# Optimization experiments

Measured on AMD Instinct MI355X. Metric: run time of the kernel, lower is better.

## Reference

```python
import jax, jax.numpy as jnp
import numpy as np

B, T, C = 1, 2048, 1024
E = 32            # n_routed_experts
TOPK = 4
H = 512           # expert_hidden_size
HS = 1024         # shared hidden: round_up(2*512, 256)
ROUTE_SCALE = 1.0


def setup_inputs() -> dict:
    key = jax.random.key(0)
    ks = jax.random.split(key, 6)
    s = 0.02  # init scale for stable logits/activations
    return {
        "x": jax.random.normal(ks[0], (B, T, C), jnp.float32),
        "gate_w": jax.random.normal(ks[1], (C, E), jnp.float32) * s,
        "gate_bias": jnp.zeros((E,), jnp.float32),
        "shared_gate_w": jax.random.normal(ks[2], (C, 2 * HS), jnp.float32) * s,
        "shared_down_w": jax.random.normal(ks[3], (HS, C), jnp.float32) * s,
        "expert_gate_w": jax.random.normal(ks[4], (E, C, 2 * H), jnp.float32) * s,
        "expert_down_w": jax.random.normal(ks[5], (E, H, C), jnp.float32) * s,
    }


def _swiglu(x, gate_w, down_w):
    # torch: y, gate = chunk(gate_proj(x), 2); down(silu(gate) * y)
    u = x @ gate_w
    y, g = jnp.split(u, 2, axis=-1)
    return (jax.nn.silu(g) * y) @ down_w


def reference(x, gate_w, gate_bias, shared_gate_w, shared_down_w,
              expert_gate_w, expert_down_w):
    Bx, Tx, Cx = x.shape
    xf = x.reshape(-1, Cx)                     # (N, C)
    N = xf.shape[0]

    # shared expert (always active)
    shared = _swiglu(x, shared_gate_w, shared_down_w)   # (B, T, C)

    # sigmoid top-k gate with load-balance bias (bias only affects selection)
    scores = jax.nn.sigmoid(xf @ gate_w)                # (N, E)
    _, topk_idx = jax.lax.top_k(scores + gate_bias, TOPK)
    w = jnp.take_along_axis(scores, topk_idx, axis=-1)  # (N, K)
    w = w / jnp.sum(w, axis=-1, keepdims=True) * ROUTE_SCALE

    # dense combine weights: combine[n, e] = routing weight of expert e for token n (0 if unselected)
    combine = jnp.zeros((N, E), xf.dtype).at[jnp.arange(N)[:, None], topk_idx].add(w)

    # routed experts: masked dense evaluation (math identical to permute + grouped GEMM + scatter-combine)
    out = jnp.zeros_like(xf)
    for e in range(E):
        out = out + combine[:, e:e + 1] * _swiglu(xf, expert_gate_w[e], expert_down_w[e])

    return shared + out.reshape(Bx, Tx, Cx)
```

## Files before the change

### kernel.cpp

```cpp
#include <hip/hip_runtime.h>
#include <hip/hip_bf16.h>
#include <math.h>

#define N_TOK 2048
#define C_DIM 1024
#define E_NUM 32
#define TOPKK 4
#define H_EXP 512
#define HS_SH 1024
#define NSLOT (N_TOK * TOPKK)

typedef __attribute__((ext_vector_type(8))) short short8;
typedef __attribute__((ext_vector_type(4))) float f32x4;

__device__ __forceinline__ ushort f2b(float f) {
    __hip_bfloat16 h = __float2bfloat16(f);
    return *(ushort*)&h;
}
__device__ __forceinline__ float silu_f(float g) { return g / (1.f + __expf(-g)); }

__device__ __forceinline__ void glds16(const ushort* g, ushort* l) {
    __builtin_amdgcn_global_load_lds(
        (const __attribute__((address_space(1))) unsigned int*)g,
        (__attribute__((address_space(3))) unsigned int*)l, 16, 0, 0);
}

__global__ __launch_bounds__(256) void router_kernel(
    const float* __restrict__ x, const float* __restrict__ gate_w,
    const float* __restrict__ gate_bias, ushort* __restrict__ xb,
    int* __restrict__ topk_idx, float* __restrict__ topk_w)
{
    __shared__ float xs[C_DIM];
    __shared__ float part[8][E_NUM];
    __shared__ float scores_s[E_NUM];
    const int n = blockIdx.x;
    const int t = threadIdx.x;
    const float* xr = x + (size_t)n * C_DIM;
    {
        float4 v = ((const float4*)xr)[t];
        xs[t * 4 + 0] = v.x; xs[t * 4 + 1] = v.y;
        xs[t * 4 + 2] = v.z; xs[t * 4 + 3] = v.w;
        ushort4 o;
        o.x = f2b(v.x); o.y = f2b(v.y); o.z = f2b(v.z); o.w = f2b(v.w);
        ((ushort4*)(xb + (size_t)n * C_DIM))[t] = o;
    }
    __syncthreads();
    const int e = t & 31, cp = t >> 5;
    float s = 0.f;
#pragma unroll 4
    for (int c = cp * 128; c < cp * 128 + 128; ++c)
        s += xs[c] * gate_w[c * E_NUM + e];
    part[cp][e] = s;
    __syncthreads();
    if (t < E_NUM) {
        float tot = 0.f;
#pragma unroll
        for (int i = 0; i < 8; ++i) tot += part[i][t];
        scores_s[t] = 1.f / (1.f + expf(-tot));
    }
    __syncthreads();
    if (t < 64) {
        const int l = t;
        const float sc  = (l < E_NUM) ? scores_s[l] : -INFINITY;
        const float scb = (l < E_NUM) ? sc + gate_bias[l] : -INFINITY;
        bool used = false;
        int myidx[TOPKK]; float myw[TOPKK]; float wsum = 0.f;
#pragma unroll
        for (int k = 0; k < TOPKK; ++k) {
            float v = used ? -INFINITY : scb;
            float m = v;
#pragma unroll
            for (int d = 1; d < 64; d <<= 1) m = fmaxf(m, __shfl_xor(m, d));
            unsigned long long b = __ballot(v == m);
            const int pick = __ffsll((unsigned long long)b) - 1;
            if (l == pick) used = true;
            const float w = __shfl(sc, pick);
            myidx[k] = pick; myw[k] = w; wsum += w;
        }
        if (l == 0) {
            const float inv = 1.0f / wsum;
#pragma unroll
            for (int k = 0; k < TOPKK; ++k) {
                topk_idx[n * TOPKK + k] = myidx[k];
                topk_w[n * TOPKK + k] = myw[k] * inv;
            }
        }
    }
}

__global__ __launch_bounds__(1024) void route_build(
    const int* __restrict__ topk_idx, const float* __restrict__ topk_w,
    int* __restrict__ offsets, int* __restrict__ perm_token,
    float* __restrict__ perm_w, int* __restrict__ inv_slot)
{
    __shared__ int cnt[E_NUM];
    __shared__ int off_s[E_NUM + 1];
    const int t = threadIdx.x;
    if (t < E_NUM) cnt[t] = 0;
    __syncthreads();
    int myidx[8];
#pragma unroll
    for (int j = 0; j < 8; ++j) {
        const int i = t * 8 + j;
        myidx[j] = topk_idx[i];
        atomicAdd(&cnt[myidx[j]], 1);
    }
    __syncthreads();
    if (t == 0) {
        int a = 0;
        for (int e2 = 0; e2 < E_NUM; ++e2) { off_s[e2] = a; a += cnt[e2]; }
        off_s[E_NUM] = a;
    }
    __syncthreads();
    if (t < E_NUM) cnt[t] = off_s[t];
    if (t <= E_NUM) offsets[t] = off_s[t];
    __syncthreads();
#pragma unroll
    for (int j = 0; j < 8; ++j) {
        const int i = t * 8 + j;
        const int pos = atomicAdd(&cnt[myidx[j]], 1);
        perm_token[pos] = i >> 2;
        perm_w[pos] = topk_w[i];
        inv_slot[i] = pos;
    }
}

template<int K, int N, int PAIR_H>
__global__ __launch_bounds__(256) void transp_conv(const float* __restrict__ in,
                                                   ushort* __restrict__ out)
{
    const float* inp = in + (size_t)blockIdx.z * K * N;
    ushort* outp = out + (size_t)blockIdx.z * K * N;
    __shared__ float T[64][65];
    const int t = threadIdx.x;
    const int k0 = blockIdx.y * 64, n0 = blockIdx.x * 64;
    {
        const int row = t >> 4;
        const int c4  = (t & 15) * 4;
#pragma unroll
        for (int i = 0; i < 4; ++i) {
            float4 v = *(const float4*)(inp + (size_t)(k0 + row + i * 16) * N + n0 + c4);
            T[row + i * 16][c4 + 0] = v.x; T[row + i * 16][c4 + 1] = v.y;
            T[row + i * 16][c4 + 2] = v.z; T[row + i * 16][c4 + 3] = v.w;
        }
    }
    __syncthreads();
    {
        const int g  = t >> 3;
        const int kg = t & 7;
#pragma unroll
        for (int p = 0; p < 2; ++p) {
            const int nn = p * 32 + g;
            const int gn = n0 + nn;
            int np;
            if (PAIR_H > 0)
                np = (gn < PAIR_H) ? ((gn >> 4) * 32 + (gn & 15))
                                   : (((gn - PAIR_H) >> 4) * 32 + 16 + ((gn - PAIR_H) & 15));
            else
                np = gn;
            short8 o;
#pragma unroll
            for (int j = 0; j < 8; ++j) o[j] = (short)f2b(T[kg * 8 + j][nn]);
            *(short8*)(outp + (size_t)np * K + k0 + kg * 8) = o;
        }
    }
}

template<int K, int NP, bool EXPERT>
__global__ __launch_bounds__(256, 3) void swiglu_mfma(
    const ushort* __restrict__ Ab, const ushort* __restrict__ Bt,
    ushort* __restrict__ Out, const int* __restrict__ offsets,
    const int* __restrict__ perm_tok)
{
    constexpr int H = NP / 2;
    int base = 0, cnt = N_TOK;
    const ushort* Bp = Bt;
    if (EXPERT) {
        const int e = blockIdx.z;
        base = offsets[e]; cnt = offsets[e + 1] - base;
        Bp = Bt + (size_t)e * NP * K;
    }
    const int m0 = blockIdx.y * 128;
    if (m0 >= cnt) return;
    const int n0 = blockIdx.x * 128;
    ushort* O = Out + (size_t)base * H;

    __shared__ __align__(16) ushort S[2 * 128 * 64];
    ushort* As = S;
    ushort* Bs = S + 128 * 64;

    const int t = threadIdx.x;
    const int lane = t & 63, wave = t >> 6;
    const int wr = wave >> 1, wc = wave & 1;
    const int quad = lane >> 4, l16 = lane & 15;
    const int srow = lane >> 3;
    const int schunk = (lane & 7) ^ srow;

    f32x4 acc[4][4];
#pragma unroll
    for (int i = 0; i < 4; ++i)
#pragma unroll
        for (int j = 0; j < 4; ++j) acc[i][j] = (f32x4){0.f, 0.f, 0.f, 0.f};

    const ushort* AgI[4];
#pragma unroll
    for (int i = 0; i < 4; ++i) {
        int ar = m0 + wave * 8 + srow + i * 32;
        if (EXPERT) {
            ar = ar < cnt ? ar : 0;
            AgI[i] = Ab + (size_t)perm_tok[base + ar] * K + schunk * 8;
        } else {
            AgI[i] = Ab + (size_t)(base + ar) * K + schunk * 8;
        }
    }
    const ushort* Bg = Bp + (size_t)(n0 + wave * 8 + srow) * K + schunk * 8;

    for (int k0 = 0; k0 < K; k0 += 64) {
        __syncthreads();
#pragma unroll
        for (int i = 0; i < 4; ++i) {
            glds16(AgI[i] + k0, As + (wave * 8 + i * 32) * 64);
            glds16(Bg + (size_t)(i * 32) * K + k0, Bs + (wave * 8 + i * 32) * 64);
        }
        __syncthreads();
#pragma unroll
        for (int ks = 0; ks < 2; ++ks) {
            const int coff = (((ks * 4 + quad) ^ (l16 & 7)) << 3);
            short8 af[4], bfr[4];
#pragma unroll
            for (int i = 0; i < 4; ++i) {
                af[i]  = *(const short8*)(As + (wr * 64 + i * 16 + l16) * 64 + coff);
                bfr[i] = *(const short8*)(Bs + (wc * 64 + i * 16 + l16) * 64 + coff);
            }
#pragma unroll
            for (int tm = 0; tm < 4; ++tm)
#pragma unroll
                for (int tn = 0; tn < 4; ++tn)
                    acc[tm][tn] = __builtin_amdgcn_mfma_f32_16x16x32_bf16(
                        af[tm], bfr[tn], acc[tm][tn], 0, 0, 0);
        }
    }

    __syncthreads();
#pragma unroll
    for (int tm = 0; tm < 4; ++tm)
#pragma unroll
        for (int p = 0; p < 2; ++p)
#pragma unroll
            for (int r = 0; r < 4; ++r) {
                const int ml = wr * 64 + tm * 16 + quad * 4 + r;
                const int hl = wc * 32 + p * 16 + l16;
                const float y = acc[tm][2 * p][r];
                const float g = acc[tm][2 * p + 1][r];
                S[ml * 72 + hl] = f2b(silu_f(g) * y);
            }
    __syncthreads();
#pragma unroll
    for (int i = 0; i < 4; ++i) {
        const int c = t + i * 256;
        const int row = c >> 3, col = (c & 7) * 8;
        if (m0 + row < cnt)
            *(float4*)(O + (size_t)(m0 + row) * H + (n0 >> 1) + col) =
                *(const float4*)(S + row * 72 + col);
    }
}

template<int K, bool EXPERT>
__global__ __launch_bounds__(256, 3) void down_mfma(
    const ushort* __restrict__ Ab, const ushort* __restrict__ Bt,
    float* __restrict__ Out, const int* __restrict__ offsets,
    const float* __restrict__ perm_w)
{
    int base = 0, cnt = N_TOK;
    const ushort* Bp = Bt;
    if (EXPERT) {
        const int e = blockIdx.z;
        base = offsets[e]; cnt = offsets[e + 1] - base;
        Bp = Bt + (size_t)e * C_DIM * K;
    }
    const int m0 = blockIdx.y * 128;
    if (m0 >= cnt) return;
    const int n0 = blockIdx.x * 128;
    const ushort* Ap = Ab + (size_t)base * K;

    __shared__ __align__(16) ushort S[2 * 128 * 64];
    ushort* As = S;
    ushort* Bs = S + 128 * 64;

    const int t = threadIdx.x;
    const int lane = t & 63, wave = t >> 6;
    const int wr = wave >> 1, wc = wave & 1;
    const int quad = lane >> 4, l16 = lane & 15;
    const int srow = lane >> 3;
    const int schunk = (lane & 7) ^ srow;

    f32x4 acc[4][4];
#pragma unroll
    for (int i = 0; i < 4; ++i)
#pragma unroll
        for (int j = 0; j < 4; ++j) acc[i][j] = (f32x4){0.f, 0.f, 0.f, 0.f};

    const ushort* Ag = Ap + (size_t)(m0 + wave * 8 + srow) * K + schunk * 8;
    const ushort* Bg = Bp + (size_t)(n0 + wave * 8 + srow) * K + schunk * 8;

    for (int k0 = 0; k0 < K; k0 += 64) {
        __syncthreads();
#pragma unroll
        for (int i = 0; i < 4; ++i) {
            glds16(Ag + (size_t)(i * 32) * K + k0, As + (wave * 8 + i * 32) * 64);
            glds16(Bg + (size_t)(i * 32) * K + k0, Bs + (wave * 8 + i * 32) * 64);
        }
        __syncthreads();
#pragma unroll
        for (int ks = 0; ks < 2; ++ks) {
            const int coff = (((ks * 4 + quad) ^ (l16 & 7)) << 3);
            short8 af[4], bfr[4];
#pragma unroll
            for (int i = 0; i < 4; ++i) {
                af[i]  = *(const short8*)(As + (wr * 64 + i * 16 + l16) * 64 + coff);
                bfr[i] = *(const short8*)(Bs + (wc * 64 + i * 16 + l16) * 64 + coff);
            }
#pragma unroll
            for (int tm = 0; tm < 4; ++tm)
#pragma unroll
                for (int tn = 0; tn < 4; ++tn)
                    acc[tm][tn] = __builtin_amdgcn_mfma_f32_16x16x32_bf16(
                        af[tm], bfr[tn], acc[tm][tn], 0, 0, 0);
        }
    }

#pragma unroll
    for (int tm = 0; tm < 4; ++tm)
#pragma unroll
        for (int r = 0; r < 4; ++r) {
            const int grow = m0 + wr * 64 + tm * 16 + quad * 4 + r;
            if (EXPERT) {
                if (grow < cnt) {
                    const float w = perm_w[base + grow];
#pragma unroll
                    for (int tn = 0; tn < 4; ++tn) {
                        const int col = n0 + wc * 64 + tn * 16 + l16;
                        Out[(size_t)(base + grow) * C_DIM + col] = w * acc[tm][tn][r];
                    }
                }
            } else {
#pragma unroll
                for (int tn = 0; tn < 4; ++tn) {
                    const int col = n0 + wc * 64 + tn * 16 + l16;
                    Out[(size_t)grow * C_DIM + col] = acc[tm][tn][r];
                }
            }
        }
}

__global__ __launch_bounds__(256) void combine_kernel(
    const float* __restrict__ Ye, const int* __restrict__ inv_slot,
    float* __restrict__ Out)
{
    const int tok = blockIdx.x;
    __shared__ int s4[TOPKK];
    if (threadIdx.x < TOPKK) s4[threadIdx.x] = inv_slot[tok * TOPKK + threadIdx.x];
    __syncthreads();
    const int c = threadIdx.x * 4;
    float4 acc = *(const float4*)(Out + (size_t)tok * C_DIM + c);
#pragma unroll
    for (int k = 0; k < TOPKK; ++k) {
        float4 v = *(const float4*)(Ye + (size_t)s4[k] * C_DIM + c);
        acc.x += v.x; acc.y += v.y; acc.z += v.z; acc.w += v.w;
    }
    *(float4*)(Out + (size_t)tok * C_DIM + c) = acc;
}

extern "C" void kernel_launch(void* const* d_in, const int* in_sizes, int n_in,
                              void* d_out, int out_size, void* d_ws, size_t ws_size,
                              hipStream_t stream)
{
    const float* x   = (const float*)d_in[0];
    const float* gw  = (const float*)d_in[1];
    const float* gb  = (const float*)d_in[2];
    const float* sgw = (const float*)d_in[3];
    const float* sdw = (const float*)d_in[4];
    const float* egw = (const float*)d_in[5];
    const float* edw = (const float*)d_in[6];
    float* out = (float*)d_out;

    char* ws = (char*)d_ws;
    size_t off = 0;
    auto alloc = [&](size_t bytes) -> void* {
        void* p = ws + off;
        off = (off + bytes + 255) & ~(size_t)255;
        return p;
    };
    int*    topk_idx = (int*)   alloc((size_t)NSLOT * sizeof(int));
    float*  topk_w   = (float*) alloc((size_t)NSLOT * sizeof(float));
    int*    offsets  = (int*)   alloc((E_NUM + 1) * sizeof(int));
    int*    perm_tok = (int*)   alloc((size_t)NSLOT * sizeof(int));
    float*  perm_w   = (float*) alloc((size_t)NSLOT * sizeof(float));
    int*    inv_slot = (int*)   alloc((size_t)NSLOT * sizeof(int));
    ushort* xb       = (ushort*)alloc((size_t)N_TOK * C_DIM * 2);
    ushort* sgw_t    = (ushort*)alloc((size_t)C_DIM * 2 * HS_SH * 2);
    ushort* sdw_t    = (ushort*)alloc((size_t)HS_SH * C_DIM * 2);
    ushort* egw_t    = (ushort*)alloc((size_t)E_NUM * C_DIM * 2 * H_EXP * 2);
    ushort* edw_t    = (ushort*)alloc((size_t)E_NUM * H_EXP * C_DIM * 2);
    ushort* Hs_b     = (ushort*)alloc((size_t)N_TOK * HS_SH * 2);
    ushort* He_b     = (ushort*)alloc((size_t)(NSLOT + 128) * H_EXP * 2);
    float*  Ye       = (float*) alloc((size_t)(NSLOT + 128) * C_DIM * sizeof(float));
    (void)ws_size; (void)in_sizes; (void)n_in; (void)out_size;

    router_kernel<<<N_TOK, 256, 0, stream>>>(x, gw, gb, xb, topk_idx, topk_w);
    route_build<<<1, 1024, 0, stream>>>(topk_idx, topk_w, offsets, perm_tok, perm_w, inv_slot);

    transp_conv<C_DIM, 2 * HS_SH, HS_SH><<<dim3(2 * HS_SH / 64, C_DIM / 64, 1), 256, 0, stream>>>(sgw, sgw_t);
    transp_conv<HS_SH, C_DIM, 0>       <<<dim3(C_DIM / 64, HS_SH / 64, 1), 256, 0, stream>>>(sdw, sdw_t);
    transp_conv<C_DIM, 2 * H_EXP, H_EXP><<<dim3(2 * H_EXP / 64, C_DIM / 64, E_NUM), 256, 0, stream>>>(egw, egw_t);
    transp_conv<H_EXP, C_DIM, 0>       <<<dim3(C_DIM / 64, H_EXP / 64, E_NUM), 256, 0, stream>>>(edw, edw_t);

    swiglu_mfma<C_DIM, 2 * HS_SH, false><<<dim3(2 * HS_SH / 128, N_TOK / 128, 1), 256, 0, stream>>>(
        xb, sgw_t, Hs_b, nullptr, nullptr);
    down_mfma<HS_SH, false><<<dim3(C_DIM / 128, N_TOK / 128, 1), 256, 0, stream>>>(
        Hs_b, sdw_t, out, nullptr, nullptr);

    swiglu_mfma<C_DIM, 2 * H_EXP, true><<<dim3(2 * H_EXP / 128, N_TOK / 128, E_NUM), 256, 0, stream>>>(
        xb, egw_t, He_b, offsets, perm_tok);
    down_mfma<H_EXP, true><<<dim3(C_DIM / 128, N_TOK / 128, E_NUM), 256, 0, stream>>>(
        He_b, edw_t, Ye, offsets, perm_w);

    combine_kernel<<<N_TOK, 256, 0, stream>>>(Ye, inv_slot, out);
}
```

Measured before the change: 429.3 us.

## Merge prep kernels and run shared/expert GEMMs in combined launches

Folds the router and the four weight transpose-convert kernels into one mega-kernel that dispatches on block index. The shared-expert and routed-expert SwiGLU GEMMs now share one launch, as do the two down GEMMs, with an extra z slice for the shared path. This removes launch gaps and tail idle time, and lets the shared and routed work fill the GPU together. In exchange, the expert z-slice of the combined launch gets 16 x-blocks, where the expert N-range only needs 8, so some blocks start and exit at once.

```diff
diff --git a/kernel.cpp b/kernel.cpp
--- a/kernel.cpp
+++ b/kernel.cpp
@@ -25,16 +25,14 @@
         (__attribute__((address_space(3))) unsigned int*)l, 16, 0, 0);
 }
 
-__global__ __launch_bounds__(256) void router_kernel(
-    const float* __restrict__ x, const float* __restrict__ gate_w,
+__device__ __forceinline__ void router_body(
+    int n, int t, const float* __restrict__ x, const float* __restrict__ gate_w,
     const float* __restrict__ gate_bias, ushort* __restrict__ xb,
-    int* __restrict__ topk_idx, float* __restrict__ topk_w)
-{
-    __shared__ float xs[C_DIM];
-    __shared__ float part[8][E_NUM];
-    __shared__ float scores_s[E_NUM];
-    const int n = blockIdx.x;
-    const int t = threadIdx.x;
+    int* __restrict__ topk_idx, float* __restrict__ topk_w, char* smem)
+{
+    float* xs = (float*)smem;
+    float (*part)[E_NUM] = (float(*)[E_NUM])(smem + 4096);
+    float* scores_s = (float*)(smem + 4096 + 1024);
     const float* xr = x + (size_t)n * C_DIM;
     {
         float4 v = ((const float4*)xr)[t];
@@ -88,52 +86,15 @@
     }
 }
 
-__global__ __launch_bounds__(1024) void route_build(
-    const int* __restrict__ topk_idx, const float* __restrict__ topk_w,
-    int* __restrict__ offsets, int* __restrict__ perm_token,
-    float* __restrict__ perm_w, int* __restrict__ inv_slot)
-{
-    __shared__ int cnt[E_NUM];
-    __shared__ int off_s[E_NUM + 1];
-    const int t = threadIdx.x;
-    if (t < E_NUM) cnt[t] = 0;
-    __syncthreads();
-    int myidx[8];
-#pragma unroll
-    for (int j = 0; j < 8; ++j) {
-        const int i = t * 8 + j;
-        myidx[j] = topk_idx[i];
-        atomicAdd(&cnt[myidx[j]], 1);
-    }
-    __syncthreads();
-    if (t == 0) {
-        int a = 0;
-        for (int e2 = 0; e2 < E_NUM; ++e2) { off_s[e2] = a; a += cnt[e2]; }
-        off_s[E_NUM] = a;
-    }
-    __syncthreads();
-    if (t < E_NUM) cnt[t] = off_s[t];
-    if (t <= E_NUM) offsets[t] = off_s[t];
-    __syncthreads();
-#pragma unroll
-    for (int j = 0; j < 8; ++j) {
-        const int i = t * 8 + j;
-        const int pos = atomicAdd(&cnt[myidx[j]], 1);
-        perm_token[pos] = i >> 2;
-        perm_w[pos] = topk_w[i];
-        inv_slot[i] = pos;
-    }
-}
-
 template<int K, int N, int PAIR_H>
-__global__ __launch_bounds__(256) void transp_conv(const float* __restrict__ in,
-                                                   ushort* __restrict__ out)
-{
-    const float* inp = in + (size_t)blockIdx.z * K * N;
-    ushort* outp = out + (size_t)blockIdx.z * K * N;
-    __shared__ float T[64][65];
-    const int t = threadIdx.x;
-    const int k0 = blockIdx.y * 64, n0 = blockIdx.x * 64;
+__device__ __forceinline__ void transp_body(const float* __restrict__ in,
+                                            ushort* __restrict__ out,
+                                            int bx, int by, int bz, int t, char* smem)
+{
+    const float* inp = in + (size_t)bz * K * N;
+    ushort* outp = out + (size_t)bz * K * N;
+    float (*T)[65] = (float(*)[65])smem;
+    const int k0 = by * 64, n0 = bx * 64;
     {
         const int row = t >> 4;
         const int c4  = (t & 15) * 4;
@@ -166,26 +127,90 @@
     }
 }
 
+__global__ __launch_bounds__(256) void prep_mega(
+    const float* __restrict__ x, const float* __restrict__ gw,
+    const float* __restrict__ gb, const float* __restrict__ sgw,
+    const float* __restrict__ sdw, const float* __restrict__ egw,
+    const float* __restrict__ edw, ushort* __restrict__ xb,
+    int* __restrict__ topk_idx, float* __restrict__ topk_w,
+    ushort* __restrict__ sgw_t, ushort* __restrict__ sdw_t,
+    ushort* __restrict__ egw_t, ushort* __restrict__ edw_t)
+{
+    __shared__ __align__(16) char smem[16640];
+    const int b = blockIdx.x;
+    const int t = threadIdx.x;
+    if (b < 512) {
+        transp_body<C_DIM, 2 * HS_SH, HS_SH>(sgw, sgw_t, b & 31, b >> 5, 0, t, smem);
+    } else if (b < 768) {
+        const int r = b - 512;
+        transp_body<HS_SH, C_DIM, 0>(sdw, sdw_t, r & 15, r >> 4, 0, t, smem);
+    } else if (b < 8960) {
+        const int r = b - 768;
+        transp_body<C_DIM, 2 * H_EXP, H_EXP>(egw, egw_t, r & 15, (r >> 4) & 15, r >> 8, t, smem);
+    } else if (b < 13056) {
+        const int r = b - 8960;
+        transp_body<H_EXP, C_DIM, 0>(edw, edw_t, r & 15, (r >> 4) & 7, r >> 7, t, smem);
+    } else {
+        router_body(b - 13056, t, x, gw, gb, xb, topk_idx, topk_w, smem);
+    }
+}
+
+__global__ __launch_bounds__(1024) void route_build(
+    const int* __restrict__ topk_idx, const float* __restrict__ topk_w,
+    int* __restrict__ offsets, int* __restrict__ perm_token,
+    float* __restrict__ perm_w, int* __restrict__ inv_slot)
+{
+    __shared__ int cnt[E_NUM];
+    __shared__ int off_s[E_NUM + 1];
+    const int t = threadIdx.x;
+    if (t < E_NUM) cnt[t] = 0;
+    __syncthreads();
+    int myidx[8];
+#pragma unroll
+    for (int j = 0; j < 8; ++j) {
+        const int i = t * 8 + j;
+        myidx[j] = topk_idx[i];
+        atomicAdd(&cnt[myidx[j]], 1);
+    }
+    __syncthreads();
+    if (t == 0) {
+        int a = 0;
+        for (int e2 = 0; e2 < E_NUM; ++e2) { off_s[e2] = a; a += cnt[e2]; }
+        off_s[E_NUM] = a;
+    }
+    __syncthreads();
+    if (t < E_NUM) cnt[t] = off_s[t];
+    if (t <= E_NUM) offsets[t] = off_s[t];
+    __syncthreads();
+#pragma unroll
+    for (int j = 0; j < 8; ++j) {
+        const int i = t * 8 + j;
+        const int pos = atomicAdd(&cnt[myidx[j]], 1);
+        perm_token[pos] = i >> 2;
+        perm_w[pos] = topk_w[i];
+        inv_slot[i] = pos;
+    }
+}
+
 template<int K, int NP, bool EXPERT>
-__global__ __launch_bounds__(256, 3) void swiglu_mfma(
+__device__ __forceinline__ void swiglu_body(
     const ushort* __restrict__ Ab, const ushort* __restrict__ Bt,
     ushort* __restrict__ Out, const int* __restrict__ offsets,
-    const int* __restrict__ perm_tok)
+    const int* __restrict__ perm_tok, int eidx, ushort* S)
 {
     constexpr int H = NP / 2;
     int base = 0, cnt = N_TOK;
     const ushort* Bp = Bt;
     if (EXPERT) {
-        const int e = blockIdx.z;
-        base = offsets[e]; cnt = offsets[e + 1] - base;
-        Bp = Bt + (size_t)e * NP * K;
-    }
+        base = offsets[eidx]; cnt = offsets[eidx + 1] - base;
+        Bp = Bt + (size_t)eidx * NP * K;
+    }
+    const int n0 = blockIdx.x * 128;
+    if (n0 >= NP) return;
     const int m0 = blockIdx.y * 128;
     if (m0 >= cnt) return;
-    const int n0 = blockIdx.x * 128;
     ushort* O = Out + (size_t)base * H;
 
-    __shared__ __align__(16) ushort S[2 * 128 * 64];
     ushort* As = S;
     ushort* Bs = S + 128 * 64;
 
@@ -266,24 +291,22 @@
 }
 
 template<int K, bool EXPERT>
-__global__ __launch_bounds__(256, 3) void down_mfma(
+__device__ __forceinline__ void down_body(
     const ushort* __restrict__ Ab, const ushort* __restrict__ Bt,
     float* __restrict__ Out, const int* __restrict__ offsets,
-    const float* __restrict__ perm_w)
+    const float* __restrict__ perm_w, int eidx, ushort* S)
 {
     int base = 0, cnt = N_TOK;
     const ushort* Bp = Bt;
     if (EXPERT) {
-        const int e = blockIdx.z;
-        base = offsets[e]; cnt = offsets[e + 1] - base;
-        Bp = Bt + (size_t)e * C_DIM * K;
+        base = offsets[eidx]; cnt = offsets[eidx + 1] - base;
+        Bp = Bt + (size_t)eidx * C_DIM * K;
     }
     const int m0 = blockIdx.y * 128;
     if (m0 >= cnt) return;
     const int n0 = blockIdx.x * 128;
     const ushort* Ap = Ab + (size_t)base * K;
 
-    __shared__ __align__(16) ushort S[2 * 128 * 64];
     ushort* As = S;
     ushort* Bs = S + 128 * 64;
 
@@ -351,6 +374,34 @@
                 }
             }
         }
+}
+
+__global__ __launch_bounds__(256, 3) void swiglu_fused(
+    const ushort* __restrict__ xb, const ushort* __restrict__ sgw_t,
+    const ushort* __restrict__ egw_t, ushort* __restrict__ Hs_b,
+    ushort* __restrict__ He_b, const int* __restrict__ offsets,
+    const int* __restrict__ perm_tok)
+{
+    __shared__ __align__(16) ushort S[2 * 128 * 64];
+    const int z = blockIdx.z;
+    if (z < E_NUM)
+        swiglu_body<C_DIM, 2 * H_EXP, true>(xb, egw_t, He_b, offsets, perm_tok, z, S);
+    else
+        swiglu_body<C_DIM, 2 * HS_SH, false>(xb, sgw_t, Hs_b, nullptr, nullptr, 0, S);
+}
+
+__global__ __launch_bounds__(256, 3) void down_fused(
+    const ushort* __restrict__ Hs_b, const ushort* __restrict__ He_b,
+    const ushort* __restrict__ sdw_t, const ushort* __restrict__ edw_t,
+    float* __restrict__ out, float* __restrict__ Ye,
+    const int* __restrict__ offsets, const float* __restrict__ perm_w)
+{
+    __shared__ __align__(16) ushort S[2 * 128 * 64];
+    const int z = blockIdx.z;
+    if (z < E_NUM)
+        down_body<H_EXP, true>(He_b, edw_t, Ye, offsets, perm_w, z, S);
+    else
+        down_body<HS_SH, false>(Hs_b, sdw_t, out, nullptr, nullptr, 0, S);
 }
 
 __global__ __launch_bounds__(256) void combine_kernel(
@@ -407,23 +458,13 @@
     float*  Ye       = (float*) alloc((size_t)(NSLOT + 128) * C_DIM * sizeof(float));
     (void)ws_size; (void)in_sizes; (void)n_in; (void)out_size;
 
-    router_kernel<<<N_TOK, 256, 0, stream>>>(x, gw, gb, xb, topk_idx, topk_w);
+    prep_mega<<<15104, 256, 0, stream>>>(x, gw, gb, sgw, sdw, egw, edw,
+                                         xb, topk_idx, topk_w,
+                                         sgw_t, sdw_t, egw_t, edw_t);
     route_build<<<1, 1024, 0, stream>>>(topk_idx, topk_w, offsets, perm_tok, perm_w, inv_slot);
-
-    transp_conv<C_DIM, 2 * HS_SH, HS_SH><<<dim3(2 * HS_SH / 64, C_DIM / 64, 1), 256, 0, stream>>>(sgw, sgw_t);
-    transp_conv<HS_SH, C_DIM, 0>       <<<dim3(C_DIM / 64, HS_SH / 64, 1), 256, 0, stream>>>(sdw, sdw_t);
-    transp_conv<C_DIM, 2 * H_EXP, H_EXP><<<dim3(2 * H_EXP / 64, C_DIM / 64, E_NUM), 256, 0, stream>>>(egw, egw_t);
-    transp_conv<H_EXP, C_DIM, 0>       <<<dim3(C_DIM / 64, H_EXP / 64, E_NUM), 256, 0, stream>>>(edw, edw_t);
-
-    swiglu_mfma<C_DIM, 2 * HS_SH, false><<<dim3(2 * HS_SH / 128, N_TOK / 128, 1), 256, 0, stream>>>(
-        xb, sgw_t, Hs_b, nullptr, nullptr);
-    down_mfma<HS_SH, false><<<dim3(C_DIM / 128, N_TOK / 128, 1), 256, 0, stream>>>(
-        Hs_b, sdw_t, out, nullptr, nullptr);
-
-    swiglu_mfma<C_DIM, 2 * H_EXP, true><<<dim3(2 * H_EXP / 128, N_TOK / 128, E_NUM), 256, 0, stream>>>(
-        xb, egw_t, He_b, offsets, perm_tok);
-    down_mfma<H_EXP, true><<<dim3(C_DIM / 128, N_TOK / 128, E_NUM), 256, 0, stream>>>(
-        He_b, edw_t, Ye, offsets, perm_w);
-
+    swiglu_fused<<<dim3(16, N_TOK / 128, E_NUM + 1), 256, 0, stream>>>(
+        xb, sgw_t, egw_t, Hs_b, He_b, offsets, perm_tok);
+    down_fused<<<dim3(C_DIM / 128, N_TOK / 128, E_NUM + 1), 256, 0, stream>>>(
+        Hs_b, He_b, sdw_t, edw_t, out, Ye, offsets, perm_w);
     combine_kernel<<<N_TOK, 256, 0, stream>>>(Ye, inv_slot, out);
 }
```

Measured after the change: 402.2 us. 6.3% less time.

## Fuse weight transpose/convert into GEMM B-staging and merge shared/expert launches

Applied to the files above, without the earlier changes.

Drops the four separate transpose-and-convert kernels. Each GEMM tile now reads the fp32 weights directly, converts them to bf16 in registers and writes them swizzled into LDS. It also merges the shared-expert and routed-expert GEMMs into single launches by using one extra grid z-slice. This removes a full pass over all the expert weights (read fp32, write bf16) and several launches. In exchange, B staging becomes strided scalar fp32 loads through registers instead of async global-to-LDS copies, and each weight tile is re-read and re-converted by every M tile.

```diff
diff --git a/kernel.cpp b/kernel.cpp
--- a/kernel.cpp
+++ b/kernel.cpp
@@ -125,67 +125,53 @@
     }
 }
 
-template<int K, int N, int PAIR_H>
-__global__ __launch_bounds__(256) void transp_conv(const float* __restrict__ in,
-                                                   ushort* __restrict__ out)
-{
-    const float* inp = in + (size_t)blockIdx.z * K * N;
-    ushort* outp = out + (size_t)blockIdx.z * K * N;
-    __shared__ float T[64][65];
-    const int t = threadIdx.x;
-    const int k0 = blockIdx.y * 64, n0 = blockIdx.x * 64;
-    {
-        const int row = t >> 4;
-        const int c4  = (t & 15) * 4;
-#pragma unroll
-        for (int i = 0; i < 4; ++i) {
-            float4 v = *(const float4*)(inp + (size_t)(k0 + row + i * 16) * N + n0 + c4);
-            T[row + i * 16][c4 + 0] = v.x; T[row + i * 16][c4 + 1] = v.y;
-            T[row + i * 16][c4 + 2] = v.z; T[row + i * 16][c4 + 3] = v.w;
-        }
-    }
-    __syncthreads();
-    {
-        const int g  = t >> 3;
-        const int kg = t & 7;
-#pragma unroll
-        for (int p = 0; p < 2; ++p) {
-            const int nn = p * 32 + g;
-            const int gn = n0 + nn;
-            int np;
-            if (PAIR_H > 0)
-                np = (gn < PAIR_H) ? ((gn >> 4) * 32 + (gn & 15))
-                                   : (((gn - PAIR_H) >> 4) * 32 + 16 + ((gn - PAIR_H) & 15));
-            else
-                np = gn;
-            short8 o;
-#pragma unroll
-            for (int j = 0; j < 8; ++j) o[j] = (short)f2b(T[kg * 8 + j][nn]);
-            *(short8*)(outp + (size_t)np * K + k0 + kg * 8) = o;
-        }
-    }
-}
-
-template<int K, int NP, bool EXPERT>
-__global__ __launch_bounds__(256, 3) void swiglu_mfma(
-    const ushort* __restrict__ Ab, const ushort* __restrict__ Bt,
+template<int NP, int PAIR_H>
+__device__ __forceinline__ void stage_B(const float* __restrict__ W, ushort* Bs,
+                                        int n0, int k0, int c, int h)
+{
+    int gn;
+    if (PAIR_H > 0) {
+        const int np = n0 + c, lo = np & 31, q = np >> 5;
+        gn = (lo < 16) ? q * 16 + lo : PAIR_H + q * 16 + (lo - 16);
+    } else {
+        gn = n0 + c;
+    }
+    const float* Wc = W + gn + (size_t)(k0 + h * 32) * NP;
+    float v[32];
+#pragma unroll
+    for (int kk = 0; kk < 32; ++kk)
+        v[kk] = Wc[(size_t)kk * NP];
+    short8 pk[4];
+#pragma unroll
+    for (int j = 0; j < 4; ++j)
+#pragma unroll
+        for (int m = 0; m < 8; ++m) pk[j][m] = (short)f2b(v[j * 8 + m]);
+#pragma unroll
+    for (int j = 0; j < 4; ++j) {
+        const int chunk = (4 * h + j) ^ (c & 7);
+        *(short8*)(Bs + c * 64 + chunk * 8) = pk[j];
+    }
+}
+
+template<int K, int NP, int PAIR_H, bool EXPERT>
+__device__ __forceinline__ void swiglu_body(
+    const ushort* __restrict__ Ab, const float* __restrict__ W,
     ushort* __restrict__ Out, const int* __restrict__ offsets,
-    const int* __restrict__ perm_tok)
+    const int* __restrict__ perm_tok, int eidx, ushort* S)
 {
     constexpr int H = NP / 2;
     int base = 0, cnt = N_TOK;
-    const ushort* Bp = Bt;
+    const float* Wp = W;
     if (EXPERT) {
-        const int e = blockIdx.z;
-        base = offsets[e]; cnt = offsets[e + 1] - base;
-        Bp = Bt + (size_t)e * NP * K;
-    }
+        base = offsets[eidx]; cnt = offsets[eidx + 1] - base;
+        Wp = W + (size_t)eidx * K * NP;
+    }
+    const int n0 = blockIdx.x * 128;
+    if (n0 >= NP) return;
     const int m0 = blockIdx.y * 128;
     if (m0 >= cnt) return;
-    const int n0 = blockIdx.x * 128;
     ushort* O = Out + (size_t)base * H;
 
-    __shared__ __align__(16) ushort S[2 * 128 * 64];
     ushort* As = S;
     ushort* Bs = S + 128 * 64;
 
@@ -195,6 +181,7 @@
     const int quad = lane >> 4, l16 = lane & 15;
     const int srow = lane >> 3;
     const int schunk = (lane & 7) ^ srow;
+    const int bc = t & 127, bh = t >> 7;
 
     f32x4 acc[4][4];
 #pragma unroll
@@ -213,15 +200,13 @@
             AgI[i] = Ab + (size_t)(base + ar) * K + schunk * 8;
         }
     }
-    const ushort* Bg = Bp + (size_t)(n0 + wave * 8 + srow) * K + schunk * 8;
 
     for (int k0 = 0; k0 < K; k0 += 64) {
         __syncthreads();
-#pragma unroll
-        for (int i = 0; i < 4; ++i) {
+        stage_B<NP, PAIR_H>(Wp, Bs, n0, k0, bc, bh);
+#pragma unroll
+        for (int i = 0; i < 4; ++i)
             glds16(AgI[i] + k0, As + (wave * 8 + i * 32) * 64);
-            glds16(Bg + (size_t)(i * 32) * K + k0, Bs + (wave * 8 + i * 32) * 64);
-        }
         __syncthreads();
 #pragma unroll
         for (int ks = 0; ks < 2; ++ks) {
@@ -266,24 +251,22 @@
 }
 
 template<int K, bool EXPERT>
-__global__ __launch_bounds__(256, 3) void down_mfma(
-    const ushort* __restrict__ Ab, const ushort* __restrict__ Bt,
+__device__ __forceinline__ void down_body(
+    const ushort* __restrict__ Ab, const float* __restrict__ W,
     float* __restrict__ Out, const int* __restrict__ offsets,
-    const float* __restrict__ perm_w)
+    const float* __restrict__ perm_w, int eidx, ushort* S)
 {
     int base = 0, cnt = N_TOK;
-    const ushort* Bp = Bt;
+    const float* Wp = W;
     if (EXPERT) {
-        const int e = blockIdx.z;
-        base = offsets[e]; cnt = offsets[e + 1] - base;
-        Bp = Bt + (size_t)e * C_DIM * K;
+        base = offsets[eidx]; cnt = offsets[eidx + 1] - base;
+        Wp = W + (size_t)eidx * K * C_DIM;
     }
     const int m0 = blockIdx.y * 128;
     if (m0 >= cnt) return;
     const int n0 = blockIdx.x * 128;
     const ushort* Ap = Ab + (size_t)base * K;
 
-    __shared__ __align__(16) ushort S[2 * 128 * 64];
     ushort* As = S;
     ushort* Bs = S + 128 * 64;
 
@@ -293,6 +276,7 @@
     const int quad = lane >> 4, l16 = lane & 15;
     const int srow = lane >> 3;
     const int schunk = (lane & 7) ^ srow;
+    const int bc = t & 127, bh = t >> 7;
 
     f32x4 acc[4][4];
 #pragma unroll
@@ -301,15 +285,13 @@
         for (int j = 0; j < 4; ++j) acc[i][j] = (f32x4){0.f, 0.f, 0.f, 0.f};
 
     const ushort* Ag = Ap + (size_t)(m0 + wave * 8 + srow) * K + schunk * 8;
-    const ushort* Bg = Bp + (size_t)(n0 + wave * 8 + srow) * K + schunk * 8;
 
     for (int k0 = 0; k0 < K; k0 += 64) {
         __syncthreads();
-#pragma unroll
-        for (int i = 0; i < 4; ++i) {
+        stage_B<C_DIM, 0>(Wp, Bs, n0, k0, bc, bh);
+#pragma unroll
+        for (int i = 0; i < 4; ++i)
             glds16(Ag + (size_t)(i * 32) * K + k0, As + (wave * 8 + i * 32) * 64);
-            glds16(Bg + (size_t)(i * 32) * K + k0, Bs + (wave * 8 + i * 32) * 64);
-        }
         __syncthreads();
 #pragma unroll
         for (int ks = 0; ks < 2; ++ks) {
@@ -351,6 +333,34 @@
                 }
             }
         }
+}
+
+__global__ __launch_bounds__(256, 3) void swiglu_fused(
+    const ushort* __restrict__ xb, const float* __restrict__ sgw,
+    const float* __restrict__ egw, ushort* __restrict__ Hs_b,
+    ushort* __restrict__ He_b, const int* __restrict__ offsets,
+    const int* __restrict__ perm_tok)
+{
+    __shared__ __align__(16) ushort S[2 * 128 * 64];
+    const int z = blockIdx.z;
+    if (z < E_NUM)
+        swiglu_body<C_DIM, 2 * H_EXP, H_EXP, true>(xb, egw, He_b, offsets, perm_tok, z, S);
+    else
+        swiglu_body<C_DIM, 2 * HS_SH, HS_SH, false>(xb, sgw, Hs_b, nullptr, nullptr, 0, S);
+}
+
+__global__ __launch_bounds__(256, 3) void down_fused(
+    const ushort* __restrict__ Hs_b, const ushort* __restrict__ He_b,
+    const float* __restrict__ sdw, const float* __restrict__ edw,
+    float* __restrict__ out, float* __restrict__ Ye,
+    const int* __restrict__ offsets, const float* __restrict__ perm_w)
+{
+    __shared__ __align__(16) ushort S[2 * 128 * 64];
+    const int z = blockIdx.z;
+    if (z < E_NUM)
+        down_body<H_EXP, true>(He_b, edw, Ye, offsets, perm_w, z, S);
+    else
+        down_body<HS_SH, false>(Hs_b, sdw, out, nullptr, nullptr, 0, S);
 }
 
 __global__ __launch_bounds__(256) void combine_kernel(
@@ -398,10 +408,6 @@
     float*  perm_w   = (float*) alloc((size_t)NSLOT * sizeof(float));
     int*    inv_slot = (int*)   alloc((size_t)NSLOT * sizeof(int));
     ushort* xb       = (ushort*)alloc((size_t)N_TOK * C_DIM * 2);
-    ushort* sgw_t    = (ushort*)alloc((size_t)C_DIM * 2 * HS_SH * 2);
-    ushort* sdw_t    = (ushort*)alloc((size_t)HS_SH * C_DIM * 2);
-    ushort* egw_t    = (ushort*)alloc((size_t)E_NUM * C_DIM * 2 * H_EXP * 2);
-    ushort* edw_t    = (ushort*)alloc((size_t)E_NUM * H_EXP * C_DIM * 2);
     ushort* Hs_b     = (ushort*)alloc((size_t)N_TOK * HS_SH * 2);
     ushort* He_b     = (ushort*)alloc((size_t)(NSLOT + 128) * H_EXP * 2);
     float*  Ye       = (float*) alloc((size_t)(NSLOT + 128) * C_DIM * sizeof(float));
@@ -409,21 +415,9 @@
 
     router_kernel<<<N_TOK, 256, 0, stream>>>(x, gw, gb, xb, topk_idx, topk_w);
     route_build<<<1, 1024, 0, stream>>>(topk_idx, topk_w, offsets, perm_tok, perm_w, inv_slot);
-
-    transp_conv<C_DIM, 2 * HS_SH, HS_SH><<<dim3(2 * HS_SH / 64, C_DIM / 64, 1), 256, 0, stream>>>(sgw, sgw_t);
-    transp_conv<HS_SH, C_DIM, 0>       <<<dim3(C_DIM / 64, HS_SH / 64, 1), 256, 0, stream>>>(sdw, sdw_t);
-    transp_conv<C_DIM, 2 * H_EXP, H_EXP><<<dim3(2 * H_EXP / 64, C_DIM / 64, E_NUM), 256, 0, stream>>>(egw, egw_t);
-    transp_conv<H_EXP, C_DIM, 0>       <<<dim3(C_DIM / 64, H_EXP / 64, E_NUM), 256, 0, stream>>>(edw, edw_t);
-
-    swiglu_mfma<C_DIM, 2 * HS_SH, false><<<dim3(2 * HS_SH / 128, N_TOK / 128, 1), 256, 0, stream>>>(
-        xb, sgw_t, Hs_b, nullptr, nullptr);
-    down_mfma<HS_SH, false><<<dim3(C_DIM / 128, N_TOK / 128, 1), 256, 0, stream>>>(
-        Hs_b, sdw_t, out, nullptr, nullptr);
-
-    swiglu_mfma<C_DIM, 2 * H_EXP, true><<<dim3(2 * H_EXP / 128, N_TOK / 128, E_NUM), 256, 0, stream>>>(
-        xb, egw_t, He_b, offsets, perm_tok);
-    down_mfma<H_EXP, true><<<dim3(C_DIM / 128, N_TOK / 128, E_NUM), 256, 0, stream>>>(
-        He_b, edw_t, Ye, offsets, perm_w);
-
+    swiglu_fused<<<dim3(16, N_TOK / 128, E_NUM + 1), 256, 0, stream>>>(
+        xb, sgw, egw, Hs_b, He_b, offsets, perm_tok);
+    down_fused<<<dim3(C_DIM / 128, N_TOK / 128, E_NUM + 1), 256, 0, stream>>>(
+        Hs_b, He_b, sdw, edw, out, Ye, offsets, perm_w);
     combine_kernel<<<N_TOK, 256, 0, stream>>>(Ye, inv_slot, out);
 }
```

After: 420.9 us. Within noise of the previous version (-2.0%).
